# Kernel tuning notes

Measured on AMD Instinct MI355X. Metric: run time of the kernel, lower is better.

Reference implementation:

```python
import jax, jax.numpy as jnp
import numpy as np

N_NODES = 50000
N_EDGES = 800000
N_FEAT = 128
N_GRAPHS = 512
OUT_DIM = 128


def gcn_conv(x, W, b, src, dst, ew, n):
    """PyG GCNConv: h = x @ W; add self-loops (weight 1); symmetric norm
    D^-1/2 A D^-1/2 with edge weights; scatter-add messages src->dst; + bias."""
    h = x @ W  # [n, out]
    loop = jnp.arange(n)
    s = jnp.concatenate([src, loop])
    d = jnp.concatenate([dst, loop])
    w = jnp.concatenate([ew, jnp.ones((n,), x.dtype)])
    deg = jax.ops.segment_sum(w, d, num_segments=n)
    dinv = jnp.where(deg > 0, jax.lax.rsqrt(deg), 0.0)
    norm = dinv[s] * w * dinv[d]  # [E+n]
    out = jax.ops.segment_sum(h[s] * norm[:, None], d, num_segments=n)
    return out + b


def setup_inputs() -> dict:
    key = jax.random.key(0)
    ks = jax.random.split(key, 12)
    F = N_FEAT
    x = jax.random.normal(ks[0], (N_NODES, F), jnp.float32)
    edge_index = jax.random.randint(ks[1], (2, N_EDGES), 0, N_NODES, jnp.int64)
    edge_attr = jax.random.uniform(ks[2], (N_EDGES,), jnp.float32)
    # deterministic sorted graph assignment -> no empty graphs (avoids -inf in max pool)
    batch = (jnp.arange(N_NODES, dtype=jnp.int64) * N_GRAPHS) // N_NODES
    def lin(k, fi, fo):
        s = 1.0 / np.sqrt(fi)
        return jax.random.uniform(k, (fi, fo), jnp.float32, -s, s)
    return {
        "x": x, "edge_attr": edge_attr,
        "W1": lin(ks[3], F, F), "b1": jnp.zeros((F,), jnp.float32),
        "W2": lin(ks[4], F, 2 * F), "b2": jnp.zeros((2 * F,), jnp.float32),
        "W3": lin(ks[5], 2 * F, 4 * F), "b3": jnp.zeros((4 * F,), jnp.float32),
        "Wf1": lin(ks[6], 4 * F, 1024), "bf1": jnp.zeros((1024,), jnp.float32),
        "Wf2": lin(ks[7], 1024, OUT_DIM), "bf2": jnp.zeros((OUT_DIM,), jnp.float32),
        "edge_index": edge_index, "batch": batch,
    }


def reference(x, edge_attr, W1, b1, W2, b2, W3, b3, Wf1, bf1, Wf2, bf2,
              edge_index, batch):
    n = x.shape[0]
    src, dst = edge_index[0], edge_index[1]
    h = jax.nn.relu(gcn_conv(x, W1, b1, src, dst, edge_attr, n))
    h = jax.nn.relu(gcn_conv(h, W2, b2, src, dst, edge_attr, n))
    h = jax.nn.relu(gcn_conv(h, W3, b3, src, dst, edge_attr, n))
    # global max pool over nodes per graph
    g = jax.ops.segment_max(h, batch, num_segments=N_GRAPHS)  # [G, 4F]
    g = jax.nn.relu(g @ Wf1 + bf1)
    # dropout is identity in eval mode
    out = g @ Wf2 + bf2
    return out
```

## Files before the change

kernel.cpp:

```cpp
#include <hip/hip_runtime.h>

#define NNODES 50000
#define NEDGES 800000
#define NGRAPH 512

typedef short bf16x8 __attribute__((ext_vector_type(8)));
typedef unsigned short u16x8 __attribute__((ext_vector_type(8)));
typedef float f32x4 __attribute__((ext_vector_type(4)));

static __device__ __forceinline__ float b2f(unsigned short u) {
    return __uint_as_float(((unsigned)u) << 16);
}
static __device__ __forceinline__ unsigned short f2b(float f) {
    unsigned u = __float_as_uint(f);
    unsigned r = (u + 0x7fffu + ((u >> 16) & 1u)) >> 16;
    return (unsigned short)r;
}

static __device__ __forceinline__ void ldrow(const unsigned short* X, size_t off, float (&v)[2]) {
    unsigned u = *(const unsigned*)(X + off);
    v[0] = b2f((unsigned short)(u & 0xffff));
    v[1] = b2f((unsigned short)(u >> 16));
}
static __device__ __forceinline__ void ldrow(const unsigned short* X, size_t off, float (&v)[4]) {
    uint2 u = *(const uint2*)(X + off);
    v[0] = b2f((unsigned short)(u.x & 0xffff));
    v[1] = b2f((unsigned short)(u.x >> 16));
    v[2] = b2f((unsigned short)(u.y & 0xffff));
    v[3] = b2f((unsigned short)(u.y >> 16));
}

__global__ void k_setup(unsigned long long* deg_cnt, int* gp) {
    int i = blockIdx.x * 256 + threadIdx.x;
    if (i < NNODES) deg_cnt[i] = (unsigned long long)(1u << 24);
    if (i < NGRAPH * 512) gp[i] = 0;
}

__global__ void k_count(const int* __restrict__ ei, const float* __restrict__ ew,
                        unsigned long long* deg_cnt) {
    int e = blockIdx.x * 256 + threadIdx.x;
    if (e < NEDGES) {
        int d = ei[NEDGES + e];
        unsigned fixed = __float2uint_rn(ew[e] * 16777216.0f);
        atomicAdd(&deg_cnt[d], ((unsigned long long)1 << 32) | fixed);
    }
}

__global__ void k_scan1(const unsigned long long* __restrict__ deg_cnt,
                        float* __restrict__ dinv,
                        int* __restrict__ ofs, int* __restrict__ bsum, int n) {
    __shared__ int wsum[4];
    const int tid = threadIdx.x, lane = tid & 63, wid = tid >> 6;
    const int idx = blockIdx.x * 256 + tid;
    int v = 0;
    if (idx < n) {
        unsigned long long dc = deg_cnt[idx];
        v = (int)(dc >> 32);
        dinv[idx] = rsqrtf((float)(unsigned)(dc & 0xffffffffull) * 5.9604645e-8f);
    }
    int s = v;
    #pragma unroll
    for (int off = 1; off < 64; off <<= 1) {
        int y = __shfl_up(s, off, 64);
        if (lane >= off) s += y;
    }
    if (lane == 63) wsum[wid] = s;
    __syncthreads();
    int waveoff = 0;
    for (int w = 0; w < wid; ++w) waveoff += wsum[w];
    if (idx < n) ofs[idx] = waveoff + s - v;
    if (tid == 255) bsum[blockIdx.x] = waveoff + s;
}
__global__ void k_scan2(int* __restrict__ bsum, int nb) {
    __shared__ int wsum[4];
    const int tid = threadIdx.x, lane = tid & 63, wid = tid >> 6;
    int v = (tid < nb) ? bsum[tid] : 0;
    int s = v;
    #pragma unroll
    for (int off = 1; off < 64; off <<= 1) {
        int y = __shfl_up(s, off, 64);
        if (lane >= off) s += y;
    }
    if (lane == 63) wsum[wid] = s;
    __syncthreads();
    int waveoff = 0;
    for (int w = 0; w < wid; ++w) waveoff += wsum[w];
    if (tid < nb) bsum[tid] = waveoff + s - v;
    if (tid == 255) bsum[nb] = waveoff + s;
}
__global__ void k_scan3(int* __restrict__ ofs, int* __restrict__ cursor,
                        const int* __restrict__ bsum, int n) {
    const int idx = blockIdx.x * 256 + threadIdx.x;
    if (idx < n) {
        int v = ofs[idx] + bsum[blockIdx.x];
        ofs[idx] = v;
        cursor[idx] = v;
    }
    if (idx == 0) ofs[n] = bsum[gridDim.x];
}

__global__ void k_fill(const int* __restrict__ ei, const float* __restrict__ ew,
                       const float* __restrict__ dinv, int* cursor,
                       unsigned long long* __restrict__ edges) {
    int e = blockIdx.x * 256 + threadIdx.x;
    if (e < NEDGES) {
        int s = ei[e];
        int d = ei[NEDGES + e];
        float c = ew[e] * dinv[s];
        int pos = atomicAdd(&cursor[d], 1);
        edges[pos] = ((unsigned long long)__float_as_uint(c) << 32) | (unsigned)s;
    }
}

__global__ void k_wt_all(const float* __restrict__ W1, const float* __restrict__ W2,
                         const float* __restrict__ W3, const float* __restrict__ Wf1,
                         const float* __restrict__ Wf2,
                         unsigned short* __restrict__ T1, unsigned short* __restrict__ T2,
                         unsigned short* __restrict__ T3, unsigned short* __restrict__ Tf1,
                         unsigned short* __restrict__ Tf2) {
    int i = blockIdx.x * 256 + threadIdx.x;
    const float* W; unsigned short* T; int K, ns;
    if (i < 16384)        { W = W1;  T = T1;  K = 128;  ns = 7;  }
    else if (i < 49152)   { W = W2;  T = T2;  K = 128;  ns = 8;  i -= 16384; }
    else if (i < 180224)  { W = W3;  T = T3;  K = 256;  ns = 9;  i -= 49152; }
    else if (i < 704512)  { W = Wf1; T = Tf1; K = 512;  ns = 10; i -= 180224; }
    else if (i < 835584)  { W = Wf2; T = Tf2; K = 1024; ns = 7;  i -= 704512; }
    else return;
    int k = i >> ns, n = i & ((1 << ns) - 1);
    T[(size_t)n * K + k] = f2b(W[i]);
}

__global__ void k_cvt4(const float* __restrict__ X, unsigned short* __restrict__ Y, int n4) {
    int i = blockIdx.x * 256 + threadIdx.x;
    if (i < n4) {
        float4 v = ((const float4*)X)[i];
        uint2 o;
        o.x = (unsigned)f2b(v.x) | ((unsigned)f2b(v.y) << 16);
        o.y = (unsigned)f2b(v.z) | ((unsigned)f2b(v.w) << 16);
        ((uint2*)Y)[i] = o;
    }
}

template <int VEC>
__global__ __launch_bounds__(256) void k_aggregate(const unsigned short* __restrict__ X,
                                                   const int* __restrict__ row_ofs,
                                                   const unsigned long long* __restrict__ edges,
                                                   const float* __restrict__ dinv,
                                                   unsigned short* __restrict__ Z) {
    const int F = 64 * VEC;
    const int wave = threadIdx.x >> 6, lane = threadIdx.x & 63;
    const int node = blockIdx.x * 4 + wave;
    if (node >= NNODES) return;
    const int fo = lane * VEC;
    const float di = dinv[node];

    float acc[VEC], v[VEC];
    ldrow(X, (size_t)node * F + fo, v);
    #pragma unroll
    for (int j = 0; j < VEC; ++j) acc[j] = di * v[j];

    int e = row_ofs[node];
    const int end = row_ofs[node + 1];
    for (; e + 8 <= end; e += 8) {
        unsigned long long pk[8];
        float vv[8][VEC];
        #pragma unroll
        for (int u = 0; u < 8; ++u) pk[u] = edges[e + u];
        #pragma unroll
        for (int u = 0; u < 8; ++u) ldrow(X, (size_t)(unsigned)pk[u] * F + fo, vv[u]);
        #pragma unroll
        for (int u = 0; u < 8; ++u) {
            float c = __uint_as_float((unsigned)(pk[u] >> 32));
            #pragma unroll
            for (int j = 0; j < VEC; ++j) acc[j] += c * vv[u][j];
        }
    }
    for (; e + 4 <= end; e += 4) {
        unsigned long long pk[4];
        float vv[4][VEC];
        #pragma unroll
        for (int u = 0; u < 4; ++u) pk[u] = edges[e + u];
        #pragma unroll
        for (int u = 0; u < 4; ++u) ldrow(X, (size_t)(unsigned)pk[u] * F + fo, vv[u]);
        #pragma unroll
        for (int u = 0; u < 4; ++u) {
            float c = __uint_as_float((unsigned)(pk[u] >> 32));
            #pragma unroll
            for (int j = 0; j < VEC; ++j) acc[j] += c * vv[u][j];
        }
    }
    for (; e < end; ++e) {
        unsigned long long pe = edges[e];
        float c = __uint_as_float((unsigned)(pe >> 32));
        ldrow(X, (size_t)(unsigned)pe * F + fo, v);
        #pragma unroll
        for (int j = 0; j < VEC; ++j) acc[j] += c * v[j];
    }

    if constexpr (VEC == 2) {
        unsigned o = (unsigned)f2b(di * acc[0]) | ((unsigned)f2b(di * acc[1]) << 16);
        *(unsigned*)(Z + (size_t)node * F + fo) = o;
    } else {
        uint2 o;
        o.x = (unsigned)f2b(di * acc[0]) | ((unsigned)f2b(di * acc[1]) << 16);
        o.y = (unsigned)f2b(di * acc[2]) | ((unsigned)f2b(di * acc[3]) << 16);
        *(uint2*)(Z + (size_t)node * F + fo) = o;
    }
}

template <int CMODE, int AFP>
__global__ __launch_bounds__(256) void k_gemm_mfma(const void* __restrict__ Av,
                                                   const unsigned short* __restrict__ WT,
                                                   const float* __restrict__ bias,
                                                   void* __restrict__ Cv,
                                                   const int* __restrict__ batch,
                                                   int* __restrict__ gp,
                                                   int M, int N, int K) {
    constexpr int LDK = 40;
    __shared__ unsigned short As[64 * LDK];
    __shared__ unsigned short Bs[128 * LDK];
    const int tid = threadIdx.x;
    const int m0 = blockIdx.y * 64, n0 = blockIdx.x * 128;
    const int wave = tid >> 6, lane = tid & 63;
    const int wm = (wave >> 1) * 32;
    const int wn = (wave & 1) * 64;
    const int quad = lane >> 4, mrow = lane & 15;

    const int ar = tid >> 2;
    const int ak = (tid & 3) * 8;
    const bool arow_ok = (m0 + ar) < M;
    const size_t aoff = (size_t)(m0 + ar) * K + ak;
    const unsigned short* Bg0 = WT + (size_t)(n0 + ar) * K + ak;
    const unsigned short* Bg1 = WT + (size_t)(n0 + ar + 64) * K + ak;

    f32x4 acc[2][4] = {};

    for (int k0 = 0; k0 < K; k0 += 32) {
        u16x8 av = {};
        if (arow_ok) {
            if constexpr (AFP) {
                const float* Af = (const float*)Av + aoff + k0;
                float4 f0 = *(const float4*)Af;
                float4 f1 = *(const float4*)(Af + 4);
                av[0] = (short)f2b(f0.x); av[1] = (short)f2b(f0.y);
                av[2] = (short)f2b(f0.z); av[3] = (short)f2b(f0.w);
                av[4] = (short)f2b(f1.x); av[5] = (short)f2b(f1.y);
                av[6] = (short)f2b(f1.z); av[7] = (short)f2b(f1.w);
            } else {
                av = *(const u16x8*)((const unsigned short*)Av + aoff + k0);
            }
        }
        u16x8 bv0 = *(const u16x8*)(Bg0 + k0);
        u16x8 bv1 = *(const u16x8*)(Bg1 + k0);
        *(u16x8*)&As[ar * LDK + ak] = av;
        *(u16x8*)&Bs[ar * LDK + ak] = bv0;
        *(u16x8*)&Bs[(ar + 64) * LDK + ak] = bv1;
        __syncthreads();
        bf16x8 af[2], bf[4];
        #pragma unroll
        for (int mt = 0; mt < 2; ++mt)
            af[mt] = *(const bf16x8*)&As[(wm + mt * 16 + mrow) * LDK + quad * 8];
        #pragma unroll
        for (int nt = 0; nt < 4; ++nt)
            bf[nt] = *(const bf16x8*)&Bs[(wn + nt * 16 + mrow) * LDK + quad * 8];
        #pragma unroll
        for (int mt = 0; mt < 2; ++mt)
            #pragma unroll
            for (int nt = 0; nt < 4; ++nt)
                acc[mt][nt] = __builtin_amdgcn_mfma_f32_16x16x32_bf16(af[mt], bf[nt], acc[mt][nt], 0, 0, 0);
        __syncthreads();
    }

    float bn[4];
    #pragma unroll
    for (int nt = 0; nt < 4; ++nt) bn[nt] = bias[n0 + wn + nt * 16 + mrow];

    if constexpr (CMODE == 0) {
        unsigned short* C = (unsigned short*)Cv;
        #pragma unroll
        for (int mt = 0; mt < 2; ++mt) {
            #pragma unroll
            for (int r = 0; r < 4; ++r) {
                int row = m0 + wm + mt * 16 + quad * 4 + r;
                if (row < M) {
                    #pragma unroll
                    for (int nt = 0; nt < 4; ++nt) {
                        float v = fmaxf(acc[mt][nt][r] + bn[nt], 0.f);
                        C[(size_t)row * N + n0 + wn + nt * 16 + mrow] = f2b(v);
                    }
                }
            }
        }
    } else if constexpr (CMODE == 1) {
        float* C = (float*)Cv;
        #pragma unroll
        for (int mt = 0; mt < 2; ++mt) {
            #pragma unroll
            for (int r = 0; r < 4; ++r) {
                int row = m0 + wm + mt * 16 + quad * 4 + r;
                if (row < M) {
                    #pragma unroll
                    for (int nt = 0; nt < 4; ++nt)
                        C[(size_t)row * N + n0 + wn + nt * 16 + mrow] = acc[mt][nt][r] + bn[nt];
                }
            }
        }
    } else {
        __shared__ float pools[2][2][128];
        const int g0 = batch[m0];
        int last = m0 + 63; if (last >= M) last = M - 1;
        const int gl = batch[last];
        int  gid[8];
        bool rok[8];
        #pragma unroll
        for (int mt = 0; mt < 2; ++mt)
            #pragma unroll
            for (int r = 0; r < 4; ++r) {
                int row = m0 + wm + mt * 16 + quad * 4 + r;
                rok[mt * 4 + r] = row < M;
                gid[mt * 4 + r] = (row < M) ? batch[row] : -1;
            }
        #pragma unroll
        for (int nt = 0; nt < 4; ++nt) {
            float v0 = 0.f, v1 = 0.f;
            #pragma unroll
            for (int mt = 0; mt < 2; ++mt)
                #pragma unroll
                for (int r = 0; r < 4; ++r) {
                    if (rok[mt * 4 + r]) {
                        float v = fmaxf(acc[mt][nt][r] + bn[nt], 0.f);
                        if (gid[mt * 4 + r] == g0) v0 = fmaxf(v0, v);
                        else v1 = fmaxf(v1, v);
                    }
                }
            v0 = fmaxf(v0, __shfl_xor(v0, 16, 64));
            v0 = fmaxf(v0, __shfl_xor(v0, 32, 64));
            v1 = fmaxf(v1, __shfl_xor(v1, 16, 64));
            v1 = fmaxf(v1, __shfl_xor(v1, 32, 64));
            if (quad == 0) {
                int c = wn + nt * 16 + mrow;
                pools[wm >> 5][0][c] = v0;
                pools[wm >> 5][1][c] = v1;
            }
        }
        __syncthreads();
        int c = tid & 127, gi = tid >> 7;
        float v = fmaxf(pools[0][gi][c], pools[1][gi][c]);
        int g = gi ? gl : g0;
        if (gi == 0 || gl != g0)
            atomicMax(&gp[(size_t)g * N + n0 + c], __float_as_int(v));
    }
}

extern "C" void kernel_launch(void* const* d_in, const int* in_sizes, int n_in,
                              void* d_out, int out_size, void* d_ws, size_t ws_size,
                              hipStream_t stream) {
    const float* x   = (const float*)d_in[0];
    const float* ew  = (const float*)d_in[1];
    const float* W1  = (const float*)d_in[2];
    const float* b1  = (const float*)d_in[3];
    const float* W2  = (const float*)d_in[4];
    const float* b2  = (const float*)d_in[5];
    const float* W3  = (const float*)d_in[6];
    const float* b3  = (const float*)d_in[7];
    const float* Wf1 = (const float*)d_in[8];
    const float* bf1 = (const float*)d_in[9];
    const float* Wf2 = (const float*)d_in[10];
    const float* bf2 = (const float*)d_in[11];
    const int* ei    = (const int*)d_in[12];
    const int* batch = (const int*)d_in[13];
    float* out = (float*)d_out;
    (void)in_sizes; (void)n_in; (void)out_size; (void)ws_size;

    char* p = (char*)d_ws;
    auto alloc = [&](size_t bytes) -> char* {
        char* r = p;
        p += (bytes + 255) & ~(size_t)255;
        return r;
    };
    const int nbN = (NNODES + 255) / 256;
    unsigned long long* deg_cnt = (unsigned long long*)alloc((size_t)NNODES * 8);
    float* dinv   = (float*)alloc((size_t)NNODES * 4);
    int*   cursor = (int*)  alloc((size_t)NNODES * 4);
    int*   rowofs = (int*)  alloc((size_t)(NNODES + 1) * 4);
    int*   bsum   = (int*)  alloc((size_t)(nbN + 1) * 4);
    unsigned long long* edges = (unsigned long long*)alloc((size_t)NEDGES * 8);
    int*   gp     = (int*)  alloc((size_t)NGRAPH * 512 * 4);
    unsigned short* f1   = (unsigned short*)alloc((size_t)NGRAPH * 1024 * 2);
    unsigned short* wt1  = (unsigned short*)alloc((size_t)128 * 128 * 2);
    unsigned short* wt2  = (unsigned short*)alloc((size_t)256 * 128 * 2);
    unsigned short* wt3  = (unsigned short*)alloc((size_t)512 * 256 * 2);
    unsigned short* wtf1 = (unsigned short*)alloc((size_t)1024 * 512 * 2);
    unsigned short* wtf2 = (unsigned short*)alloc((size_t)128 * 1024 * 2);
    unsigned short* bufA = (unsigned short*)alloc((size_t)NNODES * 256 * 2);
    unsigned short* bufB = (unsigned short*)alloc((size_t)NNODES * 256 * 2);
    unsigned short* x16  = bufB;

    const int nbE = (NEDGES + 255) / 256;
    const int MB = (NNODES + 63) / 64;
    const int AGG = (NNODES + 3) / 4;

    k_setup<<<1024, 256, 0, stream>>>(deg_cnt, gp);
    k_count<<<nbE, 256, 0, stream>>>(ei, ew, deg_cnt);
    k_scan1<<<nbN, 256, 0, stream>>>(deg_cnt, dinv, rowofs, bsum, NNODES);
    k_scan2<<<1, 256, 0, stream>>>(bsum, nbN);
    k_scan3<<<nbN, 256, 0, stream>>>(rowofs, cursor, bsum, NNODES);
    k_fill<<<nbE, 256, 0, stream>>>(ei, ew, dinv, cursor, edges);
    k_wt_all<<<(835584 + 255) / 256, 256, 0, stream>>>(W1, W2, W3, Wf1, Wf2,
                                                       wt1, wt2, wt3, wtf1, wtf2);
    k_cvt4<<<(NNODES * 128 / 4 + 255) / 256, 256, 0, stream>>>(x, x16, NNODES * 128 / 4);

    k_aggregate<2><<<AGG, 256, 0, stream>>>(x16, rowofs, edges, dinv, bufA);
    k_gemm_mfma<0, 0><<<dim3(1, MB), 256, 0, stream>>>(bufA, wt1, b1, bufB, batch, nullptr, NNODES, 128, 128);
    k_aggregate<2><<<AGG, 256, 0, stream>>>(bufB, rowofs, edges, dinv, bufA);
    k_gemm_mfma<0, 0><<<dim3(2, MB), 256, 0, stream>>>(bufA, wt2, b2, bufB, batch, nullptr, NNODES, 256, 128);
    k_aggregate<4><<<AGG, 256, 0, stream>>>(bufB, rowofs, edges, dinv, bufA);
    k_gemm_mfma<2, 0><<<dim3(4, MB), 256, 0, stream>>>(bufA, wt3, b3, nullptr, batch, gp, NNODES, 512, 256);

    k_gemm_mfma<0, 1><<<dim3(8, NGRAPH / 64), 256, 0, stream>>>(gp, wtf1, bf1, f1, batch, nullptr, NGRAPH, 1024, 512);
    k_gemm_mfma<1, 0><<<dim3(1, NGRAPH / 64), 256, 0, stream>>>(f1, wtf2, bf2, out, batch, nullptr, NGRAPH, 128, 1024);
}
```

Measured before the change: 417.9 us.

## Replace per-edge global atomic CSR fill with two-pass bucketed shared-memory sort

The CSR fill used to do one global atomicAdd per edge on a per-destination cursor and scatter randomly into memory. It now runs in two passes. The first bins edges into 196 buckets of 256 destination nodes, using shared-memory binning and one global atomic per bucket per block, and writes them into a staging buffer that reuses bufA. The second pass does a local counting sort within each bucket to place edges at their final CSR positions. The aim is to cut global atomic contention and scattered writes, at the cost of an extra pass and the staging traffic.

```diff
diff --git a/kernel.cpp b/kernel.cpp
--- a/kernel.cpp
+++ b/kernel.cpp
@@ -3,6 +3,9 @@
 #define NNODES 50000
 #define NEDGES 800000
 #define NGRAPH 512
+#define NBUCK 196
+#define FCHUNK 2048
+#define BCAP 32
 
 typedef short bf16x8 __attribute__((ext_vector_type(8)));
 typedef unsigned short u16x8 __attribute__((ext_vector_type(8)));
@@ -88,27 +91,93 @@
     if (tid < nb) bsum[tid] = waveoff + s - v;
     if (tid == 255) bsum[nb] = waveoff + s;
 }
-__global__ void k_scan3(int* __restrict__ ofs, int* __restrict__ cursor,
+__global__ void k_scan3(int* __restrict__ ofs, int* __restrict__ bcur,
                         const int* __restrict__ bsum, int n) {
     const int idx = blockIdx.x * 256 + threadIdx.x;
     if (idx < n) {
         int v = ofs[idx] + bsum[blockIdx.x];
         ofs[idx] = v;
-        cursor[idx] = v;
+        if (threadIdx.x == 0) bcur[blockIdx.x] = v;
     }
     if (idx == 0) ofs[n] = bsum[gridDim.x];
 }
 
-__global__ void k_fill(const int* __restrict__ ei, const float* __restrict__ ew,
-                       const float* __restrict__ dinv, int* cursor,
-                       unsigned long long* __restrict__ edges) {
-    int e = blockIdx.x * 256 + threadIdx.x;
-    if (e < NEDGES) {
-        int s = ei[e];
-        int d = ei[NEDGES + e];
-        float c = ew[e] * dinv[s];
-        int pos = atomicAdd(&cursor[d], 1);
-        edges[pos] = ((unsigned long long)__float_as_uint(c) << 32) | (unsigned)s;
+__global__ __launch_bounds__(256) void k_fill1(const int* __restrict__ ei,
+                                               const float* __restrict__ ew,
+                                               const float* __restrict__ dinv,
+                                               int* bcur,
+                                               unsigned long long* __restrict__ staging) {
+    __shared__ unsigned long long bin[NBUCK * BCAP];
+    __shared__ int bcnt[NBUCK];
+    const int tid = threadIdx.x;
+    if (tid < NBUCK) bcnt[tid] = 0;
+    __syncthreads();
+    const int base = blockIdx.x * FCHUNK;
+    #pragma unroll
+    for (int i = 0; i < FCHUNK / 256; ++i) {
+        int e = base + i * 256 + tid;
+        if (e < NEDGES) {
+            int s = ei[e];
+            int d = ei[NEDGES + e];
+            float c = ew[e] * dinv[s];
+            unsigned long long rec = ((unsigned long long)__float_as_uint(c) << 32)
+                                   | ((unsigned)(d & 255) << 16) | (unsigned)s;
+            int b = d >> 8;
+            int pos = atomicAdd(&bcnt[b], 1);
+            if (pos < BCAP) bin[b * BCAP + pos] = rec;
+            else staging[atomicAdd(&bcur[b], 1)] = rec;
+        }
+    }
+    __syncthreads();
+    const int wave = tid >> 6, lane = tid & 63;
+    for (int b = wave * 49; b < wave * 49 + 49; ++b) {
+        int cnt = bcnt[b]; if (cnt > BCAP) cnt = BCAP;
+        int gbase = 0;
+        if (lane == 0 && cnt > 0) gbase = atomicAdd(&bcur[b], cnt);
+        gbase = __shfl(gbase, 0, 64);
+        if (lane < cnt) staging[gbase + lane] = bin[b * BCAP + lane];
+    }
+}
+
+__global__ __launch_bounds__(256) void k_fill2(const int* __restrict__ rowofs,
+                                               const unsigned long long* __restrict__ staging,
+                                               unsigned long long* __restrict__ edges) {
+    __shared__ int cnt[256];
+    __shared__ int ofs[256];
+    __shared__ int wsum[4];
+    const int b = blockIdx.x, tid = threadIdx.x;
+    const int nbase = b * 256;
+    const int rbeg = rowofs[nbase];
+    int ntop = nbase + 256; if (ntop > NNODES) ntop = NNODES;
+    const int rend = rowofs[ntop];
+    const int c = rend - rbeg;
+    cnt[tid] = 0;
+    __syncthreads();
+    for (int i = tid; i < c; i += 256) {
+        unsigned lo = (unsigned)staging[rbeg + i];
+        atomicAdd(&cnt[(lo >> 16) & 255u], 1);
+    }
+    __syncthreads();
+    {
+        const int lane = tid & 63, wid = tid >> 6;
+        int v = cnt[tid], s = v;
+        #pragma unroll
+        for (int off = 1; off < 64; off <<= 1) {
+            int y = __shfl_up(s, off, 64);
+            if (lane >= off) s += y;
+        }
+        if (lane == 63) wsum[wid] = s;
+        __syncthreads();
+        int woff = 0;
+        for (int w = 0; w < wid; ++w) woff += wsum[w];
+        ofs[tid] = woff + s - v;
+    }
+    __syncthreads();
+    for (int i = tid; i < c; i += 256) {
+        unsigned long long rec = staging[rbeg + i];
+        unsigned lo = (unsigned)rec;
+        int slot = atomicAdd(&ofs[(lo >> 16) & 255u], 1);
+        edges[rbeg + slot] = (rec & 0xffffffff00000000ull) | (lo & 0xffffu);
     }
 }
 
@@ -381,9 +450,9 @@
     const int nbN = (NNODES + 255) / 256;
     unsigned long long* deg_cnt = (unsigned long long*)alloc((size_t)NNODES * 8);
     float* dinv   = (float*)alloc((size_t)NNODES * 4);
-    int*   cursor = (int*)  alloc((size_t)NNODES * 4);
     int*   rowofs = (int*)  alloc((size_t)(NNODES + 1) * 4);
     int*   bsum   = (int*)  alloc((size_t)(nbN + 1) * 4);
+    int*   bcur   = (int*)  alloc((size_t)NBUCK * 4);
     unsigned long long* edges = (unsigned long long*)alloc((size_t)NEDGES * 8);
     int*   gp     = (int*)  alloc((size_t)NGRAPH * 512 * 4);
     unsigned short* f1   = (unsigned short*)alloc((size_t)NGRAPH * 1024 * 2);
@@ -395,6 +464,7 @@
     unsigned short* bufA = (unsigned short*)alloc((size_t)NNODES * 256 * 2);
     unsigned short* bufB = (unsigned short*)alloc((size_t)NNODES * 256 * 2);
     unsigned short* x16  = bufB;
+    unsigned long long* staging = (unsigned long long*)bufA;
 
     const int nbE = (NEDGES + 255) / 256;
     const int MB = (NNODES + 63) / 64;
@@ -404,8 +474,9 @@
     k_count<<<nbE, 256, 0, stream>>>(ei, ew, deg_cnt);
     k_scan1<<<nbN, 256, 0, stream>>>(deg_cnt, dinv, rowofs, bsum, NNODES);
     k_scan2<<<1, 256, 0, stream>>>(bsum, nbN);
-    k_scan3<<<nbN, 256, 0, stream>>>(rowofs, cursor, bsum, NNODES);
-    k_fill<<<nbE, 256, 0, stream>>>(ei, ew, dinv, cursor, edges);
+    k_scan3<<<nbN, 256, 0, stream>>>(rowofs, bcur, bsum, NNODES);
+    k_fill1<<<(NEDGES + FCHUNK - 1) / FCHUNK, 256, 0, stream>>>(ei, ew, dinv, bcur, staging);
+    k_fill2<<<NBUCK, 256, 0, stream>>>(rowofs, staging, edges);
     k_wt_all<<<(835584 + 255) / 256, 256, 0, stream>>>(W1, W2, W3, Wf1, Wf2,
                                                        wt1, wt2, wt3, wtf1, wtf2);
     k_cvt4<<<(NNODES * 128 / 4 + 255) / 256, 256, 0, stream>>>(x, x16, NNODES * 128 / 4);
```

Result: slower. 569.2 us (+36.2%).

## Build CSR via bucketed staging and pre-scale rows by dinv

Applied to the files above, without the earlier changes.

Replaces the global degree count, three-pass scan and atomic-cursor fill with a two-level bucketing scheme. Edges are binned into 256-node buckets in staging cells, and each bucket is sorted locally in shared memory, which also computes degrees and dinv. Source-side dinv scaling moves into the feature producers (the input conversion and the GEMM epilogue), so edge coefficients no longer need a dinv gather. This cuts several launches and scattered global atomics, but adds a spill path, a 16-bit node-id packing that depends on the node count, and extra rounding from storing pre-scaled bf16 features.

```diff
diff --git a/kernel.cpp b/kernel.cpp
--- a/kernel.cpp
+++ b/kernel.cpp
@@ -3,10 +3,14 @@
 #define NNODES 50000
 #define NEDGES 800000
 #define NGRAPH 512
+#define NBUCK 196
+#define NCELL (NBUCK * 8)
+#define CAP 896
 
 typedef short bf16x8 __attribute__((ext_vector_type(8)));
 typedef unsigned short u16x8 __attribute__((ext_vector_type(8)));
 typedef float f32x4 __attribute__((ext_vector_type(4)));
+typedef unsigned long long u64;
 
 static __device__ __forceinline__ float b2f(unsigned short u) {
     return __uint_as_float(((unsigned)u) << 16);
@@ -30,35 +34,41 @@
     v[3] = b2f((unsigned short)(u.y >> 16));
 }
 
-__global__ void k_setup(unsigned long long* deg_cnt, int* gp) {
+__global__ void k_setup(int* gp, int* cur, int* spillcnt) {
     int i = blockIdx.x * 256 + threadIdx.x;
-    if (i < NNODES) deg_cnt[i] = (unsigned long long)(1u << 24);
     if (i < NGRAPH * 512) gp[i] = 0;
-}
-
-__global__ void k_count(const int* __restrict__ ei, const float* __restrict__ ew,
-                        unsigned long long* deg_cnt) {
+    if (i < NCELL) cur[i] = 0;
+    if (i == 0) *spillcnt = 0;
+}
+
+__global__ void k_bucket(const int* __restrict__ ei, const float* __restrict__ ew,
+                         int* cur, u64* __restrict__ staging,
+                         u64* __restrict__ spill, int* spillcnt) {
     int e = blockIdx.x * 256 + threadIdx.x;
     if (e < NEDGES) {
+        int s = ei[e];
         int d = ei[NEDGES + e];
-        unsigned fixed = __float2uint_rn(ew[e] * 16777216.0f);
-        atomicAdd(&deg_cnt[d], ((unsigned long long)1 << 32) | fixed);
-    }
-}
-
-__global__ void k_scan1(const unsigned long long* __restrict__ deg_cnt,
-                        float* __restrict__ dinv,
-                        int* __restrict__ ofs, int* __restrict__ bsum, int n) {
+        float w = ew[e];
+        int b = d >> 8;
+        int cell = b * 8 + (blockIdx.x & 7);
+        unsigned lo = ((unsigned)b << 24) | ((unsigned)(d & 255) << 16) | (unsigned)s;
+        u64 rec = ((u64)__float_as_uint(w) << 32) | lo;
+        int pos = atomicAdd(&cur[cell], 1);
+        if (pos < CAP) staging[(size_t)cell * CAP + pos] = rec;
+        else spill[atomicAdd(spillcnt, 1)] = rec;
+    }
+}
+
+__global__ void k_bscan(const int* __restrict__ cur, int* __restrict__ bucketbase,
+                        int* __restrict__ rowofs) {
     __shared__ int wsum[4];
     const int tid = threadIdx.x, lane = tid & 63, wid = tid >> 6;
-    const int idx = blockIdx.x * 256 + tid;
-    int v = 0;
-    if (idx < n) {
-        unsigned long long dc = deg_cnt[idx];
-        v = (int)(dc >> 32);
-        dinv[idx] = rsqrtf((float)(unsigned)(dc & 0xffffffffull) * 5.9604645e-8f);
-    }
-    int s = v;
+    int tot = 0;
+    if (tid < NBUCK) {
+        #pragma unroll
+        for (int c = 0; c < 8; ++c) tot += cur[tid * 8 + c];
+    }
+    int s = tot;
     #pragma unroll
     for (int off = 1; off < 64; off <<= 1) {
         int y = __shfl_up(s, off, 64);
@@ -66,49 +76,93 @@
     }
     if (lane == 63) wsum[wid] = s;
     __syncthreads();
-    int waveoff = 0;
-    for (int w = 0; w < wid; ++w) waveoff += wsum[w];
-    if (idx < n) ofs[idx] = waveoff + s - v;
-    if (tid == 255) bsum[blockIdx.x] = waveoff + s;
-}
-__global__ void k_scan2(int* __restrict__ bsum, int nb) {
+    int woff = 0;
+    for (int w = 0; w < wid; ++w) woff += wsum[w];
+    if (tid < NBUCK) bucketbase[tid] = woff + s - tot;
+    if (tid == 255) { bucketbase[NBUCK] = woff + s; rowofs[NNODES] = woff + s; }
+}
+
+__global__ __launch_bounds__(256) void k_fill2(const int* __restrict__ cur,
+                                               const int* __restrict__ bucketbase,
+                                               const u64* __restrict__ staging,
+                                               const u64* __restrict__ spill,
+                                               const int* __restrict__ spillcnt,
+                                               int* __restrict__ rowofs,
+                                               float* __restrict__ dinv,
+                                               u64* __restrict__ edges) {
+    __shared__ float degs[256];
+    __shared__ int cnt[256];
+    __shared__ int lofs[256];
     __shared__ int wsum[4];
-    const int tid = threadIdx.x, lane = tid & 63, wid = tid >> 6;
-    int v = (tid < nb) ? bsum[tid] : 0;
-    int s = v;
+    const int b = blockIdx.x, tid = threadIdx.x;
+    cnt[tid] = 0;
+    degs[tid] = 1.0f;
+    __syncthreads();
     #pragma unroll
-    for (int off = 1; off < 64; off <<= 1) {
-        int y = __shfl_up(s, off, 64);
-        if (lane >= off) s += y;
-    }
-    if (lane == 63) wsum[wid] = s;
+    for (int c = 0; c < 8; ++c) {
+        int cell = b * 8 + c;
+        int len = cur[cell]; if (len > CAP) len = CAP;
+        for (int i = tid; i < len; i += 256) {
+            u64 rec = staging[(size_t)cell * CAP + i];
+            unsigned lo = (unsigned)rec;
+            int n = (lo >> 16) & 255;
+            atomicAdd(&cnt[n], 1);
+            atomicAdd(&degs[n], __uint_as_float((unsigned)(rec >> 32)));
+        }
+    }
+    const int sp = *spillcnt;
+    for (int i = tid; i < sp; i += 256) {
+        u64 rec = spill[i];
+        unsigned lo = (unsigned)rec;
+        if ((int)(lo >> 24) == b) {
+            int n = (lo >> 16) & 255;
+            atomicAdd(&cnt[n], 1);
+            atomicAdd(&degs[n], __uint_as_float((unsigned)(rec >> 32)));
+        }
+    }
     __syncthreads();
-    int waveoff = 0;
-    for (int w = 0; w < wid; ++w) waveoff += wsum[w];
-    if (tid < nb) bsum[tid] = waveoff + s - v;
-    if (tid == 255) bsum[nb] = waveoff + s;
-}
-__global__ void k_scan3(int* __restrict__ ofs, int* __restrict__ cursor,
-                        const int* __restrict__ bsum, int n) {
-    const int idx = blockIdx.x * 256 + threadIdx.x;
-    if (idx < n) {
-        int v = ofs[idx] + bsum[blockIdx.x];
-        ofs[idx] = v;
-        cursor[idx] = v;
-    }
-    if (idx == 0) ofs[n] = bsum[gridDim.x];
-}
-
-__global__ void k_fill(const int* __restrict__ ei, const float* __restrict__ ew,
-                       const float* __restrict__ dinv, int* cursor,
-                       unsigned long long* __restrict__ edges) {
-    int e = blockIdx.x * 256 + threadIdx.x;
-    if (e < NEDGES) {
-        int s = ei[e];
-        int d = ei[NEDGES + e];
-        float c = ew[e] * dinv[s];
-        int pos = atomicAdd(&cursor[d], 1);
-        edges[pos] = ((unsigned long long)__float_as_uint(c) << 32) | (unsigned)s;
+    {
+        const int lane = tid & 63, wid = tid >> 6;
+        int v = cnt[tid], s = v;
+        #pragma unroll
+        for (int off = 1; off < 64; off <<= 1) {
+            int y = __shfl_up(s, off, 64);
+            if (lane >= off) s += y;
+        }
+        if (lane == 63) wsum[wid] = s;
+        __syncthreads();
+        int woff = 0;
+        for (int w = 0; w < wid; ++w) woff += wsum[w];
+        lofs[tid] = woff + s - v;
+    }
+    __syncthreads();
+    const int base = bucketbase[b];
+    const int node = b * 256 + tid;
+    if (node < NNODES) {
+        rowofs[node] = base + lofs[tid];
+        dinv[node] = rsqrtf(degs[tid]);
+    }
+    __syncthreads();
+    #pragma unroll
+    for (int c = 0; c < 8; ++c) {
+        int cell = b * 8 + c;
+        int len = cur[cell]; if (len > CAP) len = CAP;
+        for (int i = tid; i < len; i += 256) {
+            u64 rec = staging[(size_t)cell * CAP + i];
+            unsigned lo = (unsigned)rec;
+            int n = (lo >> 16) & 255;
+            int slot = atomicAdd(&lofs[n], 1);
+            edges[base + slot] = (rec & 0xffffffff00000000ull) | (lo & 0xffffu);
+        }
+    }
+    for (int i = tid; i < sp; i += 256) {
+        u64 rec = spill[i];
+        unsigned lo = (unsigned)rec;
+        if ((int)(lo >> 24) == b) {
+            int n = (lo >> 16) & 255;
+            int slot = atomicAdd(&lofs[n], 1);
+            edges[base + slot] = (rec & 0xffffffff00000000ull) | (lo & 0xffffu);
+        }
     }
 }
 
@@ -130,13 +184,15 @@
     T[(size_t)n * K + k] = f2b(W[i]);
 }
 
-__global__ void k_cvt4(const float* __restrict__ X, unsigned short* __restrict__ Y, int n4) {
+__global__ void k_cvt4(const float* __restrict__ X, const float* __restrict__ dinv,
+                       unsigned short* __restrict__ Y, int n4) {
     int i = blockIdx.x * 256 + threadIdx.x;
     if (i < n4) {
         float4 v = ((const float4*)X)[i];
+        float d = dinv[i >> 5];
         uint2 o;
-        o.x = (unsigned)f2b(v.x) | ((unsigned)f2b(v.y) << 16);
-        o.y = (unsigned)f2b(v.z) | ((unsigned)f2b(v.w) << 16);
+        o.x = (unsigned)f2b(v.x * d) | ((unsigned)f2b(v.y * d) << 16);
+        o.y = (unsigned)f2b(v.z * d) | ((unsigned)f2b(v.w * d) << 16);
         ((uint2*)Y)[i] = o;
     }
 }
@@ -144,7 +200,7 @@
 template <int VEC>
 __global__ __launch_bounds__(256) void k_aggregate(const unsigned short* __restrict__ X,
                                                    const int* __restrict__ row_ofs,
-                                                   const unsigned long long* __restrict__ edges,
+                                                   const u64* __restrict__ edges,
                                                    const float* __restrict__ dinv,
                                                    unsigned short* __restrict__ Z) {
     const int F = 64 * VEC;
@@ -157,17 +213,17 @@
     float acc[VEC], v[VEC];
     ldrow(X, (size_t)node * F + fo, v);
     #pragma unroll
-    for (int j = 0; j < VEC; ++j) acc[j] = di * v[j];
+    for (int j = 0; j < VEC; ++j) acc[j] = v[j];
 
     int e = row_ofs[node];
     const int end = row_ofs[node + 1];
     for (; e + 8 <= end; e += 8) {
-        unsigned long long pk[8];
+        u64 pk[8];
         float vv[8][VEC];
         #pragma unroll
         for (int u = 0; u < 8; ++u) pk[u] = edges[e + u];
         #pragma unroll
-        for (int u = 0; u < 8; ++u) ldrow(X, (size_t)(unsigned)pk[u] * F + fo, vv[u]);
+        for (int u = 0; u < 8; ++u) ldrow(X, (size_t)(unsigned)(pk[u] & 0xffffu) * F + fo, vv[u]);
         #pragma unroll
         for (int u = 0; u < 8; ++u) {
             float c = __uint_as_float((unsigned)(pk[u] >> 32));
@@ -176,12 +232,12 @@
         }
     }
     for (; e + 4 <= end; e += 4) {
-        unsigned long long pk[4];
+        u64 pk[4];
         float vv[4][VEC];
         #pragma unroll
         for (int u = 0; u < 4; ++u) pk[u] = edges[e + u];
         #pragma unroll
-        for (int u = 0; u < 4; ++u) ldrow(X, (size_t)(unsigned)pk[u] * F + fo, vv[u]);
+        for (int u = 0; u < 4; ++u) ldrow(X, (size_t)(unsigned)(pk[u] & 0xffffu) * F + fo, vv[u]);
         #pragma unroll
         for (int u = 0; u < 4; ++u) {
             float c = __uint_as_float((unsigned)(pk[u] >> 32));
@@ -190,9 +246,9 @@
         }
     }
     for (; e < end; ++e) {
-        unsigned long long pe = edges[e];
+        u64 pe = edges[e];
         float c = __uint_as_float((unsigned)(pe >> 32));
-        ldrow(X, (size_t)(unsigned)pe * F + fo, v);
+        ldrow(X, (size_t)(unsigned)(pe & 0xffffu) * F + fo, v);
         #pragma unroll
         for (int j = 0; j < VEC; ++j) acc[j] += c * v[j];
     }
@@ -215,6 +271,7 @@
                                                    void* __restrict__ Cv,
                                                    const int* __restrict__ batch,
                                                    int* __restrict__ gp,
+                                                   const float* __restrict__ rscale,
                                                    int M, int N, int K) {
     constexpr int LDK = 40;
     __shared__ unsigned short As[64 * LDK];
@@ -283,9 +340,10 @@
             for (int r = 0; r < 4; ++r) {
                 int row = m0 + wm + mt * 16 + quad * 4 + r;
                 if (row < M) {
+                    float rs = rscale ? rscale[row] : 1.0f;
                     #pragma unroll
                     for (int nt = 0; nt < 4; ++nt) {
-                        float v = fmaxf(acc[mt][nt][r] + bn[nt], 0.f);
+                        float v = fmaxf(acc[mt][nt][r] + bn[nt], 0.f) * rs;
                         C[(size_t)row * N + n0 + wn + nt * 16 + mrow] = f2b(v);
                     }
                 }
@@ -378,13 +436,13 @@
         p += (bytes + 255) & ~(size_t)255;
         return r;
     };
-    const int nbN = (NNODES + 255) / 256;
-    unsigned long long* deg_cnt = (unsigned long long*)alloc((size_t)NNODES * 8);
     float* dinv   = (float*)alloc((size_t)NNODES * 4);
-    int*   cursor = (int*)  alloc((size_t)NNODES * 4);
     int*   rowofs = (int*)  alloc((size_t)(NNODES + 1) * 4);
-    int*   bsum   = (int*)  alloc((size_t)(nbN + 1) * 4);
-    unsigned long long* edges = (unsigned long long*)alloc((size_t)NEDGES * 8);
+    int*   bbase  = (int*)  alloc((size_t)(NBUCK + 1) * 4);
+    int*   cur    = (int*)  alloc((size_t)NCELL * 4);
+    int*   spillc = (int*)  alloc(4);
+    u64*   spill  = (u64*)  alloc((size_t)4096 * 8);
+    u64*   edges  = (u64*)  alloc((size_t)NEDGES * 8);
     int*   gp     = (int*)  alloc((size_t)NGRAPH * 512 * 4);
     unsigned short* f1   = (unsigned short*)alloc((size_t)NGRAPH * 1024 * 2);
     unsigned short* wt1  = (unsigned short*)alloc((size_t)128 * 128 * 2);
@@ -395,28 +453,27 @@
     unsigned short* bufA = (unsigned short*)alloc((size_t)NNODES * 256 * 2);
     unsigned short* bufB = (unsigned short*)alloc((size_t)NNODES * 256 * 2);
     unsigned short* x16  = bufB;
+    u64* staging = (u64*)bufA;
 
     const int nbE = (NEDGES + 255) / 256;
     const int MB = (NNODES + 63) / 64;
     const int AGG = (NNODES + 3) / 4;
 
-    k_setup<<<1024, 256, 0, stream>>>(deg_cnt, gp);
-    k_count<<<nbE, 256, 0, stream>>>(ei, ew, deg_cnt);
-    k_scan1<<<nbN, 256, 0, stream>>>(deg_cnt, dinv, rowofs, bsum, NNODES);
-    k_scan2<<<1, 256, 0, stream>>>(bsum, nbN);
-    k_scan3<<<nbN, 256, 0, stream>>>(rowofs, cursor, bsum, NNODES);
-    k_fill<<<nbE, 256, 0, stream>>>(ei, ew, dinv, cursor, edges);
+    k_setup<<<1024, 256, 0, stream>>>(gp, cur, spillc);
+    k_bucket<<<nbE, 256, 0, stream>>>(ei, ew, cur, staging, spill, spillc);
+    k_bscan<<<1, 256, 0, stream>>>(cur, bbase, rowofs);
+    k_fill2<<<NBUCK, 256, 0, stream>>>(cur, bbase, staging, spill, spillc, rowofs, dinv, edges);
     k_wt_all<<<(835584 + 255) / 256, 256, 0, stream>>>(W1, W2, W3, Wf1, Wf2,
                                                        wt1, wt2, wt3, wtf1, wtf2);
-    k_cvt4<<<(NNODES * 128 / 4 + 255) / 256, 256, 0, stream>>>(x, x16, NNODES * 128 / 4);
+    k_cvt4<<<(NNODES * 32 + 255) / 256, 256, 0, stream>>>(x, dinv, x16, NNODES * 32);
 
     k_aggregate<2><<<AGG, 256, 0, stream>>>(x16, rowofs, edges, dinv, bufA);
-    k_gemm_mfma<0, 0><<<dim3(1, MB), 256, 0, stream>>>(bufA, wt1, b1, bufB, batch, nullptr, NNODES, 128, 128);
+    k_gemm_mfma<0, 0><<<dim3(1, MB), 256, 0, stream>>>(bufA, wt1, b1, bufB, batch, nullptr, dinv, NNODES, 128, 128);
     k_aggregate<2><<<AGG, 256, 0, stream>>>(bufB, rowofs, edges, dinv, bufA);
-    k_gemm_mfma<0, 0><<<dim3(2, MB), 256, 0, stream>>>(bufA, wt2, b2, bufB, batch, nullptr, NNODES, 256, 128);
+    k_gemm_mfma<0, 0><<<dim3(2, MB), 256, 0, stream>>>(bufA, wt2, b2, bufB, batch, nullptr, dinv, NNODES, 256, 128);
     k_aggregate<4><<<AGG, 256, 0, stream>>>(bufB, rowofs, edges, dinv, bufA);
-    k_gemm_mfma<2, 0><<<dim3(4, MB), 256, 0, stream>>>(bufA, wt3, b3, nullptr, batch, gp, NNODES, 512, 256);
-
-    k_gemm_mfma<0, 1><<<dim3(8, NGRAPH / 64), 256, 0, stream>>>(gp, wtf1, bf1, f1, batch, nullptr, NGRAPH, 1024, 512);
-    k_gemm_mfma<1, 0><<<dim3(1, NGRAPH / 64), 256, 0, stream>>>(f1, wtf2, bf2, out, batch, nullptr, NGRAPH, 128, 1024);
-}
+    k_gemm_mfma<2, 0><<<dim3(4, MB), 256, 0, stream>>>(bufA, wt3, b3, nullptr, batch, gp, nullptr, NNODES, 512, 256);
+
+    k_gemm_mfma<0, 1><<<dim3(8, NGRAPH / 64), 256, 0, stream>>>(gp, wtf1, bf1, f1, batch, nullptr, nullptr, NGRAPH, 1024, 512);
+    k_gemm_mfma<1, 0><<<dim3(1, NGRAPH / 64), 256, 0, stream>>>(f1, wtf2, bf2, out, batch, nullptr, nullptr, NGRAPH, 128, 1024);
+}
```

Measured after the change: 486.1 us. +16.3%, slower.

## Compact CSR edges to 32-bit and fold source normalization into node features

Applied to the files above, without the earlier changes.

The count pass now records each edge's arrival order from the degree atomic. The fill pass uses that order to place edges without a second atomic cursor. Each edge record shrinks from 64 to 32 bits: a 16-bit source index plus the raw edge weight in bf16. The dinv[s] factor moves out of the edge data and into the node features, applied in the input conversion and in the GEMM epilogues through a new row-scale argument. This cuts edge-stream bandwidth in the three aggregations and removes atomics from the fill. The cost is an extra seq buffer, reliance on fewer than 65536 nodes, and bf16 rounding of edge weights.

```diff
diff --git a/kernel.cpp b/kernel.cpp
--- a/kernel.cpp
+++ b/kernel.cpp
@@ -7,6 +7,7 @@
 typedef short bf16x8 __attribute__((ext_vector_type(8)));
 typedef unsigned short u16x8 __attribute__((ext_vector_type(8)));
 typedef float f32x4 __attribute__((ext_vector_type(4)));
+typedef unsigned long long u64;
 
 static __device__ __forceinline__ float b2f(unsigned short u) {
     return __uint_as_float(((unsigned)u) << 16);
@@ -30,31 +31,31 @@
     v[3] = b2f((unsigned short)(u.y >> 16));
 }
 
-__global__ void k_setup(unsigned long long* deg_cnt, int* gp) {
+__global__ void k_setup(u64* deg_cnt, int* gp) {
     int i = blockIdx.x * 256 + threadIdx.x;
-    if (i < NNODES) deg_cnt[i] = (unsigned long long)(1u << 24);
+    if (i < NNODES) deg_cnt[i] = (u64)(1u << 24);
     if (i < NGRAPH * 512) gp[i] = 0;
 }
 
 __global__ void k_count(const int* __restrict__ ei, const float* __restrict__ ew,
-                        unsigned long long* deg_cnt) {
+                        u64* deg_cnt, int* __restrict__ seq) {
     int e = blockIdx.x * 256 + threadIdx.x;
     if (e < NEDGES) {
         int d = ei[NEDGES + e];
         unsigned fixed = __float2uint_rn(ew[e] * 16777216.0f);
-        atomicAdd(&deg_cnt[d], ((unsigned long long)1 << 32) | fixed);
-    }
-}
-
-__global__ void k_scan1(const unsigned long long* __restrict__ deg_cnt,
-                        float* __restrict__ dinv,
+        u64 old = atomicAdd(&deg_cnt[d], ((u64)1 << 32) | fixed);
+        seq[e] = (int)(old >> 32);
+    }
+}
+
+__global__ void k_scan1(const u64* __restrict__ deg_cnt, float* __restrict__ dinv,
                         int* __restrict__ ofs, int* __restrict__ bsum, int n) {
     __shared__ int wsum[4];
     const int tid = threadIdx.x, lane = tid & 63, wid = tid >> 6;
     const int idx = blockIdx.x * 256 + tid;
     int v = 0;
     if (idx < n) {
-        unsigned long long dc = deg_cnt[idx];
+        u64 dc = deg_cnt[idx];
         v = (int)(dc >> 32);
         dinv[idx] = rsqrtf((float)(unsigned)(dc & 0xffffffffull) * 5.9604645e-8f);
     }
@@ -88,27 +89,21 @@
     if (tid < nb) bsum[tid] = waveoff + s - v;
     if (tid == 255) bsum[nb] = waveoff + s;
 }
-__global__ void k_scan3(int* __restrict__ ofs, int* __restrict__ cursor,
-                        const int* __restrict__ bsum, int n) {
+__global__ void k_scan3(int* __restrict__ ofs, const int* __restrict__ bsum, int n) {
     const int idx = blockIdx.x * 256 + threadIdx.x;
-    if (idx < n) {
-        int v = ofs[idx] + bsum[blockIdx.x];
-        ofs[idx] = v;
-        cursor[idx] = v;
-    }
+    if (idx < n) ofs[idx] += bsum[blockIdx.x];
     if (idx == 0) ofs[n] = bsum[gridDim.x];
 }
 
 __global__ void k_fill(const int* __restrict__ ei, const float* __restrict__ ew,
-                       const float* __restrict__ dinv, int* cursor,
-                       unsigned long long* __restrict__ edges) {
+                       const int* __restrict__ seq, const int* __restrict__ rowofs,
+                       unsigned* __restrict__ edges) {
     int e = blockIdx.x * 256 + threadIdx.x;
     if (e < NEDGES) {
         int s = ei[e];
         int d = ei[NEDGES + e];
-        float c = ew[e] * dinv[s];
-        int pos = atomicAdd(&cursor[d], 1);
-        edges[pos] = ((unsigned long long)__float_as_uint(c) << 32) | (unsigned)s;
+        int pos = rowofs[d] + seq[e];
+        edges[pos] = ((unsigned)f2b(ew[e]) << 16) | (unsigned)s;
     }
 }
 
@@ -130,13 +125,15 @@
     T[(size_t)n * K + k] = f2b(W[i]);
 }
 
-__global__ void k_cvt4(const float* __restrict__ X, unsigned short* __restrict__ Y, int n4) {
+__global__ void k_cvt4(const float* __restrict__ X, const float* __restrict__ dinv,
+                       unsigned short* __restrict__ Y, int n4) {
     int i = blockIdx.x * 256 + threadIdx.x;
     if (i < n4) {
         float4 v = ((const float4*)X)[i];
+        float d = dinv[i >> 5];
         uint2 o;
-        o.x = (unsigned)f2b(v.x) | ((unsigned)f2b(v.y) << 16);
-        o.y = (unsigned)f2b(v.z) | ((unsigned)f2b(v.w) << 16);
+        o.x = (unsigned)f2b(v.x * d) | ((unsigned)f2b(v.y * d) << 16);
+        o.y = (unsigned)f2b(v.z * d) | ((unsigned)f2b(v.w * d) << 16);
         ((uint2*)Y)[i] = o;
     }
 }
@@ -144,7 +141,7 @@
 template <int VEC>
 __global__ __launch_bounds__(256) void k_aggregate(const unsigned short* __restrict__ X,
                                                    const int* __restrict__ row_ofs,
-                                                   const unsigned long long* __restrict__ edges,
+                                                   const unsigned* __restrict__ edges,
                                                    const float* __restrict__ dinv,
                                                    unsigned short* __restrict__ Z) {
     const int F = 64 * VEC;
@@ -157,42 +154,42 @@
     float acc[VEC], v[VEC];
     ldrow(X, (size_t)node * F + fo, v);
     #pragma unroll
-    for (int j = 0; j < VEC; ++j) acc[j] = di * v[j];
+    for (int j = 0; j < VEC; ++j) acc[j] = v[j];
 
     int e = row_ofs[node];
     const int end = row_ofs[node + 1];
     for (; e + 8 <= end; e += 8) {
-        unsigned long long pk[8];
+        unsigned pk[8];
         float vv[8][VEC];
         #pragma unroll
         for (int u = 0; u < 8; ++u) pk[u] = edges[e + u];
         #pragma unroll
-        for (int u = 0; u < 8; ++u) ldrow(X, (size_t)(unsigned)pk[u] * F + fo, vv[u]);
+        for (int u = 0; u < 8; ++u) ldrow(X, (size_t)(pk[u] & 0xffffu) * F + fo, vv[u]);
         #pragma unroll
         for (int u = 0; u < 8; ++u) {
-            float c = __uint_as_float((unsigned)(pk[u] >> 32));
+            float c = b2f((unsigned short)(pk[u] >> 16));
             #pragma unroll
             for (int j = 0; j < VEC; ++j) acc[j] += c * vv[u][j];
         }
     }
     for (; e + 4 <= end; e += 4) {
-        unsigned long long pk[4];
+        unsigned pk[4];
         float vv[4][VEC];
         #pragma unroll
         for (int u = 0; u < 4; ++u) pk[u] = edges[e + u];
         #pragma unroll
-        for (int u = 0; u < 4; ++u) ldrow(X, (size_t)(unsigned)pk[u] * F + fo, vv[u]);
+        for (int u = 0; u < 4; ++u) ldrow(X, (size_t)(pk[u] & 0xffffu) * F + fo, vv[u]);
         #pragma unroll
         for (int u = 0; u < 4; ++u) {
-            float c = __uint_as_float((unsigned)(pk[u] >> 32));
+            float c = b2f((unsigned short)(pk[u] >> 16));
             #pragma unroll
             for (int j = 0; j < VEC; ++j) acc[j] += c * vv[u][j];
         }
     }
     for (; e < end; ++e) {
-        unsigned long long pe = edges[e];
-        float c = __uint_as_float((unsigned)(pe >> 32));
-        ldrow(X, (size_t)(unsigned)pe * F + fo, v);
+        unsigned pe = edges[e];
+        float c = b2f((unsigned short)(pe >> 16));
+        ldrow(X, (size_t)(pe & 0xffffu) * F + fo, v);
         #pragma unroll
         for (int j = 0; j < VEC; ++j) acc[j] += c * v[j];
     }
@@ -215,6 +212,7 @@
                                                    void* __restrict__ Cv,
                                                    const int* __restrict__ batch,
                                                    int* __restrict__ gp,
+                                                   const float* __restrict__ rscale,
                                                    int M, int N, int K) {
     constexpr int LDK = 40;
     __shared__ unsigned short As[64 * LDK];
@@ -283,9 +281,10 @@
             for (int r = 0; r < 4; ++r) {
                 int row = m0 + wm + mt * 16 + quad * 4 + r;
                 if (row < M) {
+                    float rs = rscale ? rscale[row] : 1.0f;
                     #pragma unroll
                     for (int nt = 0; nt < 4; ++nt) {
-                        float v = fmaxf(acc[mt][nt][r] + bn[nt], 0.f);
+                        float v = fmaxf(acc[mt][nt][r] + bn[nt], 0.f) * rs;
                         C[(size_t)row * N + n0 + wn + nt * 16 + mrow] = f2b(v);
                     }
                 }
@@ -379,12 +378,12 @@
         return r;
     };
     const int nbN = (NNODES + 255) / 256;
-    unsigned long long* deg_cnt = (unsigned long long*)alloc((size_t)NNODES * 8);
+    u64*   deg_cnt = (u64*)alloc((size_t)NNODES * 8);
     float* dinv   = (float*)alloc((size_t)NNODES * 4);
-    int*   cursor = (int*)  alloc((size_t)NNODES * 4);
+    int*   seq    = (int*)  alloc((size_t)NEDGES * 4);
     int*   rowofs = (int*)  alloc((size_t)(NNODES + 1) * 4);
     int*   bsum   = (int*)  alloc((size_t)(nbN + 1) * 4);
-    unsigned long long* edges = (unsigned long long*)alloc((size_t)NEDGES * 8);
+    unsigned* edges = (unsigned*)alloc((size_t)NEDGES * 4);
     int*   gp     = (int*)  alloc((size_t)NGRAPH * 512 * 4);
     unsigned short* f1   = (unsigned short*)alloc((size_t)NGRAPH * 1024 * 2);
     unsigned short* wt1  = (unsigned short*)alloc((size_t)128 * 128 * 2);
@@ -401,22 +400,22 @@
     const int AGG = (NNODES + 3) / 4;
 
     k_setup<<<1024, 256, 0, stream>>>(deg_cnt, gp);
-    k_count<<<nbE, 256, 0, stream>>>(ei, ew, deg_cnt);
+    k_count<<<nbE, 256, 0, stream>>>(ei, ew, deg_cnt, seq);
     k_scan1<<<nbN, 256, 0, stream>>>(deg_cnt, dinv, rowofs, bsum, NNODES);
     k_scan2<<<1, 256, 0, stream>>>(bsum, nbN);
-    k_scan3<<<nbN, 256, 0, stream>>>(rowofs, cursor, bsum, NNODES);
-    k_fill<<<nbE, 256, 0, stream>>>(ei, ew, dinv, cursor, edges);
+    k_scan3<<<nbN, 256, 0, stream>>>(rowofs, bsum, NNODES);
+    k_fill<<<nbE, 256, 0, stream>>>(ei, ew, seq, rowofs, edges);
     k_wt_all<<<(835584 + 255) / 256, 256, 0, stream>>>(W1, W2, W3, Wf1, Wf2,
                                                        wt1, wt2, wt3, wtf1, wtf2);
-    k_cvt4<<<(NNODES * 128 / 4 + 255) / 256, 256, 0, stream>>>(x, x16, NNODES * 128 / 4);
+    k_cvt4<<<(NNODES * 32 + 255) / 256, 256, 0, stream>>>(x, dinv, x16, NNODES * 32);
 
     k_aggregate<2><<<AGG, 256, 0, stream>>>(x16, rowofs, edges, dinv, bufA);
-    k_gemm_mfma<0, 0><<<dim3(1, MB), 256, 0, stream>>>(bufA, wt1, b1, bufB, batch, nullptr, NNODES, 128, 128);
+    k_gemm_mfma<0, 0><<<dim3(1, MB), 256, 0, stream>>>(bufA, wt1, b1, bufB, batch, nullptr, dinv, NNODES, 128, 128);
     k_aggregate<2><<<AGG, 256, 0, stream>>>(bufB, rowofs, edges, dinv, bufA);
-    k_gemm_mfma<0, 0><<<dim3(2, MB), 256, 0, stream>>>(bufA, wt2, b2, bufB, batch, nullptr, NNODES, 256, 128);
+    k_gemm_mfma<0, 0><<<dim3(2, MB), 256, 0, stream>>>(bufA, wt2, b2, bufB, batch, nullptr, dinv, NNODES, 256, 128);
     k_aggregate<4><<<AGG, 256, 0, stream>>>(bufB, rowofs, edges, dinv, bufA);
-    k_gemm_mfma<2, 0><<<dim3(4, MB), 256, 0, stream>>>(bufA, wt3, b3, nullptr, batch, gp, NNODES, 512, 256);
-
-    k_gemm_mfma<0, 1><<<dim3(8, NGRAPH / 64), 256, 0, stream>>>(gp, wtf1, bf1, f1, batch, nullptr, NGRAPH, 1024, 512);
-    k_gemm_mfma<1, 0><<<dim3(1, NGRAPH / 64), 256, 0, stream>>>(f1, wtf2, bf2, out, batch, nullptr, NGRAPH, 128, 1024);
-}
+    k_gemm_mfma<2, 0><<<dim3(4, MB), 256, 0, stream>>>(bufA, wt3, b3, nullptr, batch, gp, nullptr, NNODES, 512, 256);
+
+    k_gemm_mfma<0, 1><<<dim3(8, NGRAPH / 64), 256, 0, stream>>>(gp, wtf1, bf1, f1, batch, nullptr, nullptr, NGRAPH, 1024, 512);
+    k_gemm_mfma<1, 0><<<dim3(1, NGRAPH / 64), 256, 0, stream>>>(f1, wtf2, bf2, out, batch, nullptr, nullptr, NGRAPH, 128, 1024);
+}
```

New measurement: 381.5 us. 1.1x faster.
